# Performance work log

Measured on AMD Instinct MI355X. Metric: run time of the kernel, lower is better.

Reference implementation:

```python
import jax, jax.numpy as jnp
import numpy as np

B, N, D = 4, 8192, 512
L, W, S = 64, 64, 32  # num_tokens, win_size, stride


def setup_inputs() -> dict:
    key = jax.random.key(0)
    ks = jax.random.split(key, 12)
    inp = {
        "feats": jax.random.normal(ks[0], (B, N, D), jnp.float32),
        "coords": jax.random.normal(ks[1], (B, N, 2), jnp.float32) * 100.0,
        "mask": jnp.zeros((B, N), dtype=bool),
        "z": jax.random.normal(ks[2], (L, D), jnp.float32) * 0.02,
        "Wq": jax.random.normal(ks[3], (D, D), jnp.float32) * 0.01,
        "Wk": jax.random.normal(ks[4], (D, D), jnp.float32) * 0.01,
        "Wv": jax.random.normal(ks[5], (D, D), jnp.float32) * 0.01,
        "W1": jax.random.normal(ks[6], (D, 2), jnp.float32) * 0.05,
        "b1": jnp.zeros((D,), jnp.float32),
        "W2": jax.random.normal(ks[7], (D, D), jnp.float32) * 0.01,
        "b2": jnp.zeros((D,), jnp.float32),
        "Wo": jax.random.normal(ks[8], (D, D), jnp.float32) * 0.01,
        "bo": jnp.zeros((D,), jnp.float32),
    }
    return inp


def reference(feats, coords, mask, z, Wq, Wk, Wv, W1, b1, W2, b2, Wo, bo):
    # mask is all-False: every token valid, N_valid == N, segments are
    # contiguous blocks of P = N // L tokens (seg_id = floor(i*L/N)).
    Bz, Nn, Dd = feats.shape
    Ll = z.shape[0]
    P = Nn // Ll  # tokens per segment

    # LayerNorm over feature dim (no affine, eps=1e-5 as in F.layer_norm)
    mu = feats.mean(-1, keepdims=True)
    var = feats.var(-1, keepdims=True)
    f_ln = (feats - mu) * jax.lax.rsqrt(var + 1e-5)

    # per-sample coordinate normalization (torch std is unbiased, ddof=1)
    c_mu = coords.mean(1, keepdims=True)
    c_sd = coords.std(1, keepdims=True, ddof=1) + 1e-8
    c_n = (coords - c_mu) / c_sd

    f_seg = f_ln.reshape(Bz, Ll, P, Dd)
    c_seg = c_n.reshape(Bz, Ll, P, 2)

    # static sliding windows within each segment (last window may be partial)
    starts = np.arange(0, P, S)                      # [nw]
    idx = starts[:, None] + np.arange(W)[None, :]    # [nw, W]
    valid = jnp.asarray(idx < P)                     # [nw, W] bool
    idx_c = np.minimum(idx, P - 1)
    cnt = valid.sum(-1).astype(feats.dtype)          # [nw]

    f_win = f_seg[:, :, idx_c]                       # [B,L,nw,W,D]
    c_win = c_seg[:, :, idx_c]                       # [B,L,nw,W,2]

    vmask = valid.astype(feats.dtype)[None, None, :, :, None]
    c_mean = (c_win * vmask).sum(3) / cnt[None, None, :, None]   # [B,L,nw,2]
    pos_in = c_win - c_mean[:, :, :, None, :]
    h = jax.nn.relu(jnp.einsum('blnwc,dc->blnwd', pos_in, W1) + b1)
    pos_bias = jnp.einsum('blnwd,ed->blnwe', h, W2) + b2

    q = z @ Wq.T                                     # [L,D]
    k = jnp.einsum('blnwd,ed->blnwe', f_win, Wk) + pos_bias
    v = jnp.einsum('blnwd,ed->blnwe', f_win, Wv)

    temperature = jnp.sqrt(jnp.asarray(Dd, feats.dtype))
    logits = jnp.einsum('ld,blnwd->blnw', q, k) / temperature
    logits = jnp.clip(logits, -10.0, 10.0)
    logits = jnp.where(valid[None, None], logits, -jnp.inf)
    attn = jax.nn.softmax(logits, axis=-1)           # [B,L,nw,W]

    z_win = jnp.einsum('blnw,blnwd->blnd', attn, v)  # [B,L,nw,D]
    z_l = z_win.mean(2)                              # average over windows
    return z_l @ Wo.T + bo                           # [B,L,D]
```

## Files before the change

kernel.cpp:

```cpp
#include <hip/hip_runtime.h>

#define Bz 4
#define Nn 8192
#define Dd 512
#define Ll 64
#define Pp 128
#define Ww 64
#define Ss 32
#define NW 4

__global__ __launch_bounds__(256) void pre_k(
    const float* __restrict__ coords,
    const float* __restrict__ z,  const float* __restrict__ Wq,
    const float* __restrict__ Wk, const float* __restrict__ W2,
    const float* __restrict__ b2,
    const float* __restrict__ Wv, const float* __restrict__ Wo,
    float* __restrict__ cstats,
    float* __restrict__ QK, float* __restrict__ G,
    float* __restrict__ sqk4, float* __restrict__ qb2,
    float* __restrict__ WvoT) {
    __shared__ float smem[64 * 68 + 64 * 36];
    int bid = blockIdx.x, tid = threadIdx.x;
    int wv = tid >> 6, lane = tid & 63;

    if (bid < 256) {
        int l = bid & 63, ch = bid >> 6;
        float* qs  = smem;
        float* pq  = smem + 512;
        float* pg  = smem + 1536;
        float* red = smem + 2560;

        float zr[8];
        {
            const float4* zp = (const float4*)&z[(size_t)l * Dd + lane * 8];
            float4 z0 = zp[0], z1 = zp[1];
            zr[0] = z0.x; zr[1] = z0.y; zr[2] = z0.z; zr[3] = z0.w;
            zr[4] = z1.x; zr[5] = z1.y; zr[6] = z1.z; zr[7] = z1.w;
        }
        for (int i = 0; i < 128; i += 2) {
            int d0 = wv * 128 + i;
            const float4* r0 = (const float4*)&Wq[(size_t)d0 * Dd];
            const float4* r1 = (const float4*)&Wq[(size_t)(d0 + 1) * Dd];
            float4 a0 = r0[lane * 2], a1 = r0[lane * 2 + 1];
            float4 b0 = r1[lane * 2], b1 = r1[lane * 2 + 1];
            float s0 = a0.x * zr[0] + a0.y * zr[1] + a0.z * zr[2] + a0.w * zr[3]
                     + a1.x * zr[4] + a1.y * zr[5] + a1.z * zr[6] + a1.w * zr[7];
            float s1 = b0.x * zr[0] + b0.y * zr[1] + b0.z * zr[2] + b0.w * zr[3]
                     + b1.x * zr[4] + b1.y * zr[5] + b1.z * zr[6] + b1.w * zr[7];
            for (int o = 32; o > 0; o >>= 1) { s0 += __shfl_xor(s0, o); s1 += __shfl_xor(s1, o); }
            if (lane == 0) { qs[d0] = s0; qs[d0 + 1] = s1; }
        }
        __syncthreads();
        if (ch == 0) {
            float p = qs[tid] * b2[tid] + qs[tid + 256] * b2[tid + 256];
            for (int o = 32; o > 0; o >>= 1) p += __shfl_xor(p, o);
            if (lane == 0) red[4 + wv] = p;
        }
        {
            int qd = tid & 31, h = tid >> 5;
            int cb = ch * 128 + qd * 4;
            float4 aq = make_float4(0.f, 0.f, 0.f, 0.f);
            float4 ag = make_float4(0.f, 0.f, 0.f, 0.f);
            for (int e = h * 64; e < h * 64 + 64; ++e) {
                float qe = qs[e];
                float4 wk = *(const float4*)&Wk[(size_t)e * Dd + cb];
                float4 w2 = *(const float4*)&W2[(size_t)e * Dd + cb];
                aq.x = fmaf(qe, wk.x, aq.x); aq.y = fmaf(qe, wk.y, aq.y);
                aq.z = fmaf(qe, wk.z, aq.z); aq.w = fmaf(qe, wk.w, aq.w);
                ag.x = fmaf(qe, w2.x, ag.x); ag.y = fmaf(qe, w2.y, ag.y);
                ag.z = fmaf(qe, w2.z, ag.z); ag.w = fmaf(qe, w2.w, ag.w);
            }
            *(float4*)&pq[h * 128 + qd * 4] = aq;
            *(float4*)&pg[h * 128 + qd * 4] = ag;
        }
        __syncthreads();
        if (tid < 128) {
            float vq = 0.f, vg = 0.f;
#pragma unroll
            for (int hh = 0; hh < 8; ++hh) { vq += pq[hh * 128 + tid]; vg += pg[hh * 128 + tid]; }
            QK[(size_t)l * Dd + ch * 128 + tid] = vq;
            G [(size_t)l * Dd + ch * 128 + tid] = vg;
            float s = vq;
            for (int o = 32; o > 0; o >>= 1) s += __shfl_xor(s, o);
            if (lane == 0) red[wv] = s;
        }
        __syncthreads();
        if (tid == 0) sqk4[ch * 64 + l] = red[0] + red[1];
        if (ch == 0 && tid == 32) qb2[l] = red[4] + red[5] + red[6] + red[7];
    } else if (bid < 384) {
        int wb = bid - 256;
        int m0 = (wb >> 4) * 64;
        int n0 = (wb & 15) * 32;
        float (*As)[68] = (float (*)[68])smem;
        float (*Bs)[36] = (float (*)[36])(smem + 64 * 68);
        int tx = tid & 31, ty = tid >> 5;
        float acc[8] = {0.f, 0.f, 0.f, 0.f, 0.f, 0.f, 0.f, 0.f};
        for (int c0 = 0; c0 < Dd; c0 += 64) {
            int r = tid >> 4, c4 = (tid & 15) * 4;
#pragma unroll
            for (int i = 0; i < 4; ++i) {
                int cc = r + 16 * i;
                float4 v = *(const float4*)&Wv[(size_t)(c0 + cc) * Dd + m0 + c4];
                As[c4 + 0][cc] = v.x; As[c4 + 1][cc] = v.y;
                As[c4 + 2][cc] = v.z; As[c4 + 3][cc] = v.w;
            }
#pragma unroll
            for (int i = 0; i < 2; ++i) {
                int nn = r + 16 * i;
                float4 v = *(const float4*)&Wo[(size_t)(n0 + nn) * Dd + c0 + c4];
                Bs[c4 + 0][nn] = v.x; Bs[c4 + 1][nn] = v.y;
                Bs[c4 + 2][nn] = v.z; Bs[c4 + 3][nn] = v.w;
            }
            __syncthreads();
#pragma unroll 16
            for (int kk = 0; kk < 64; ++kk) {
                float bv = Bs[kk][tx];
#pragma unroll
                for (int i = 0; i < 8; ++i)
                    acc[i] = fmaf(As[ty + 8 * i][kk], bv, acc[i]);
            }
            __syncthreads();
        }
#pragma unroll
        for (int i = 0; i < 8; ++i)
            WvoT[(size_t)(m0 + ty + 8 * i) * Dd + n0 + tx] = acc[i];
    } else {
        int b = bid - 384;
        double sx = 0, sy = 0, sxx = 0, syy = 0;
        const float4* cp = (const float4*)(coords + (size_t)b * Nn * 2);
        for (int i = tid; i < Nn / 2; i += 256) {
            float4 v = cp[i];
            sx  += (double)v.x + (double)v.z;
            sy  += (double)v.y + (double)v.w;
            sxx += (double)v.x * v.x + (double)v.z * v.z;
            syy += (double)v.y * v.y + (double)v.w * v.w;
        }
        for (int o = 32; o > 0; o >>= 1) {
            sx  += __shfl_down(sx,  o); sy  += __shfl_down(sy,  o);
            sxx += __shfl_down(sxx, o); syy += __shfl_down(syy, o);
        }
        double* dred = (double*)smem;
        if (lane == 0) {
            dred[wv * 4 + 0] = sx;  dred[wv * 4 + 1] = sy;
            dred[wv * 4 + 2] = sxx; dred[wv * 4 + 3] = syy;
        }
        __syncthreads();
        if (tid == 0) {
            double tx = 0, ty = 0, txx = 0, tyy = 0;
            for (int i = 0; i < 4; ++i) {
                tx += dred[i * 4 + 0]; ty += dred[i * 4 + 1];
                txx += dred[i * 4 + 2]; tyy += dred[i * 4 + 3];
            }
            const double N = (double)Nn;
            double mux = tx / N, muy = ty / N;
            double vx = (txx - N * mux * mux) / (N - 1.0);
            double vy = (tyy - N * muy * muy) / (N - 1.0);
            cstats[b * 4 + 0] = (float)mux;
            cstats[b * 4 + 1] = (float)muy;
            cstats[b * 4 + 2] = (float)sqrt(vx) + 1e-8f;
            cstats[b * 4 + 3] = (float)sqrt(vy) + 1e-8f;
        }
    }
}

__global__ __launch_bounds__(512) void attn2(
    const float* __restrict__ feats, const float* __restrict__ coords,
    const float* __restrict__ cstats,
    const float* __restrict__ QKm, const float* __restrict__ Gm,
    const float* __restrict__ sqk4, const float* __restrict__ qb2,
    const float* __restrict__ W1, const float* __restrict__ b1,
    const float* __restrict__ WvoT, const float* __restrict__ bo,
    float* __restrict__ out) {
    __shared__ float  qk_s[Dd];
    __shared__ float4 wpack[Dd];
    __shared__ float  scx[Pp], scy[Pp];
    __shared__ float  smu[Pp], srs[Pp], sa[Pp];
    __shared__ float  shs[NW * Ww];
    __shared__ float  sar[NW][Ww];
    __shared__ float  swt[Pp];
    __shared__ float  scm[8];
    __shared__ float  s2red[NW];
    __shared__ float  soff;
    __shared__ float  spart[4][Dd];
    __shared__ float  fm_s[Dd];

    int bx = blockIdx.x;
    int l = bx & 63, b = bx >> 6;
    int tid = threadIdx.x;
    int wv = tid >> 6, lane = tid & 63;

    qk_s[tid]  = QKm[l * Dd + tid];
    wpack[tid] = make_float4(W1[2 * tid], W1[2 * tid + 1], b1[tid], Gm[l * Dd + tid]);
    if (tid < Pp) {
        int row = bx * Pp + tid;
        float x = coords[(size_t)row * 2], y = coords[(size_t)row * 2 + 1];
        scx[tid] = (x - cstats[b * 4 + 0]) / cstats[b * 4 + 2];
        scy[tid] = (y - cstats[b * 4 + 1]) / cstats[b * 4 + 3];
    }
    float sqk_l = sqk4[l] + sqk4[64 + l] + sqk4[128 + l] + sqk4[192 + l];
    float qb2_l = qb2[l];
    __syncthreads();

    if (wv < 4) {
        int n = wv, w = lane;
        int nv = (n == 3) ? 32 : 64;
        float cx = (w < nv) ? scx[n * Ss + w] : 0.f;
        float cy = (w < nv) ? scy[n * Ss + w] : 0.f;
        for (int o = 32; o > 0; o >>= 1) { cx += __shfl_xor(cx, o); cy += __shfl_xor(cy, o); }
        if (lane == 0) { scm[n] = cx / (float)nv; scm[4 + n] = cy / (float)nv; }
    }

    const float* fbase = feats + (size_t)bx * Pp * Dd;
    float4 q0 = ((const float4*)qk_s)[lane];
    float4 q1 = ((const float4*)qk_s)[lane + 64];
#pragma unroll 2
    for (int i = 0; i < 16; ++i) {
        int r = wv * 16 + i;
        const float4* fr = (const float4*)(fbase + (size_t)r * Dd);
        float4 v0 = fr[lane];
        float4 v1 = fr[lane + 64];
        float s  = v0.x + v0.y + v0.z + v0.w + v1.x + v1.y + v1.z + v1.w;
        float ss = v0.x * v0.x + v0.y * v0.y + v0.z * v0.z + v0.w * v0.w
                 + v1.x * v1.x + v1.y * v1.y + v1.z * v1.z + v1.w * v1.w;
        float a  = v0.x * q0.x + v0.y * q0.y + v0.z * q0.z + v0.w * q0.w
                 + v1.x * q1.x + v1.y * q1.y + v1.z * q1.z + v1.w * q1.w;
        for (int o = 32; o > 0; o >>= 1) {
            s += __shfl_xor(s, o); ss += __shfl_xor(ss, o); a += __shfl_xor(a, o);
        }
        if (lane == 0) {
            float mu  = s * (1.f / (float)Dd);
            float var = ss * (1.f / (float)Dd) - mu * mu;
            smu[r] = mu; srs[r] = 1.f / sqrtf(var + 1e-5f); sa[r] = a;
        }
    }
    __syncthreads();

    {
        int s = tid >> 1, half = tid & 1;
        int n = s >> 6, w = s & 63;
        int nv = (n == 3) ? 32 : 64;
        float hs = 0.f;
        if (w < nv) {
            int p = n * Ss + w;
            float px = scx[p] - scm[n], py = scy[p] - scm[4 + n];
            int d0 = half * 256;
#pragma unroll 4
            for (int d = d0; d < d0 + 256; ++d) {
                float4 c = wpack[d];
                hs = fmaf(c.w, fmaxf(fmaf(c.x, px, fmaf(c.y, py, c.z)), 0.f), hs);
            }
        }
        hs += __shfl_xor(hs, 1);
        if (half == 0) shs[s] = hs;
    }
    __syncthreads();

    const float invtemp = 0.04419417382415922f;
    if (wv < 4) {
        int n = wv, w = lane;
        int nv = (n == 3) ? 32 : 64;
        int p = n * Ss + ((w < nv) ? w : 0);
        float lg = -1e30f;
        if (w < nv) {
            lg = (srs[p] * (sa[p] - smu[p] * sqk_l) + shs[n * Ww + w] + qb2_l) * invtemp;
            lg = fminf(fmaxf(lg, -10.f), 10.f);
        }
        float m = lg;
        for (int o = 32; o > 0; o >>= 1) m = fmaxf(m, __shfl_xor(m, o));
        float e = (w < nv) ? expf(lg - m) : 0.f;
        float ssum = e;
        for (int o = 32; o > 0; o >>= 1) ssum += __shfl_xor(ssum, o);
        float ar = (w < nv) ? (e / ssum) * srs[p] : 0.f;
        sar[n][w] = ar;
        float t2 = (w < nv) ? ar * smu[p] : 0.f;
        for (int o = 32; o > 0; o >>= 1) t2 += __shfl_xor(t2, o);
        if (lane == 0) s2red[n] = t2;
    }
    __syncthreads();

    if (tid < Pp) {
        int p = tid;
        int na = (p >> 5) - 1, nb = (p >> 5);
        float wt = 0.f;
        if (na >= 0 && na <= 3) wt += sar[na][p - na * Ss];
        if (nb <= 3)            wt += sar[nb][p - nb * Ss];
        swt[p] = wt;
    }
    if (tid == 0) soff = 0.25f * (s2red[0] + s2red[1] + s2red[2] + s2red[3]);
    __syncthreads();

    {
        int g = tid >> 7, c4 = tid & 127;
        const float4* f4 = (const float4*)fbase;
        float4 acc = make_float4(0.f, 0.f, 0.f, 0.f);
#pragma unroll 4
        for (int p = g; p < Pp; p += 4) {
            float wt = swt[p];
            float4 v = f4[p * 128 + c4];
            acc.x = fmaf(wt, v.x, acc.x);
            acc.y = fmaf(wt, v.y, acc.y);
            acc.z = fmaf(wt, v.z, acc.z);
            acc.w = fmaf(wt, v.w, acc.w);
        }
        *(float4*)&spart[g][c4 * 4] = acc;
    }
    __syncthreads();
    fm_s[tid] = 0.25f * (spart[0][tid] + spart[1][tid] + spart[2][tid] + spart[3][tid]) - soff;
    __syncthreads();

    {
        int cq = (tid & 127) * 4, h = tid >> 7;
        float4 acc = make_float4(0.f, 0.f, 0.f, 0.f);
#pragma unroll 4
        for (int e = h * 128; e < h * 128 + 128; ++e) {
            float fe = fm_s[e];
            float4 w = *(const float4*)&WvoT[(size_t)e * Dd + cq];
            acc.x = fmaf(fe, w.x, acc.x);
            acc.y = fmaf(fe, w.y, acc.y);
            acc.z = fmaf(fe, w.z, acc.z);
            acc.w = fmaf(fe, w.w, acc.w);
        }
        *(float4*)&spart[h][cq] = acc;
    }
    __syncthreads();
    out[(size_t)bx * Dd + tid] = bo[tid]
        + spart[0][tid] + spart[1][tid] + spart[2][tid] + spart[3][tid];
}

extern "C" void kernel_launch(void* const* d_in, const int* in_sizes, int n_in,
                              void* d_out, int out_size, void* d_ws, size_t ws_size,
                              hipStream_t stream) {
    const float* feats  = (const float*)d_in[0];
    const float* coords = (const float*)d_in[1];
    const float* z  = (const float*)d_in[3];
    const float* Wq = (const float*)d_in[4];
    const float* Wk = (const float*)d_in[5];
    const float* Wv = (const float*)d_in[6];
    const float* W1 = (const float*)d_in[7];
    const float* b1 = (const float*)d_in[8];
    const float* W2 = (const float*)d_in[9];
    const float* b2 = (const float*)d_in[10];
    const float* Wo = (const float*)d_in[11];
    const float* bo = (const float*)d_in[12];
    float* out = (float*)d_out;

    float* ws = (float*)d_ws;
    float* cstats = ws;
    float* QK     = ws + 16;
    float* G      = QK + Ll * Dd;
    float* sqk4   = G + Ll * Dd;
    float* qb2    = sqk4 + 256;
    float* WvoT   = qb2 + Ll;

    pre_k<<<388, 256, 0, stream>>>(coords, z, Wq, Wk, W2, b2, Wv, Wo,
                                   cstats, QK, G, sqk4, qb2, WvoT);

    attn2<<<Bz * Ll, 512, 0, stream>>>(feats, coords, cstats,
                                       QK, G, sqk4, qb2, W1, b1,
                                       WvoT, bo, out);
}
```

Before: 183.9 us.

## Precompute Wq·Wk and Wq·W2 products, keep feature rows in registers

The query-key projection is re-associated. Instead of computing q = z·Wq^T per token and then q·Wk, pre1 builds the weight products Wq^T·Wk, Wq^T·W2 and b2·Wq in tiled GEMM blocks, and a new qkg_k kernel applies z to them. In attn2 each block loads its 128×512 feature slab into registers once and reuses it for both the LayerNorm/dot pass and the weighted-sum pass, so the second global read of feats goes away. This adds a third launch and a large per-thread register footprint, which risks spills or lower occupancy.

New measurement: 199.6 us. 1.09x slower.

```diff
diff --git a/kernel.cpp b/kernel.cpp
--- a/kernel.cpp
+++ b/kernel.cpp
@@ -9,107 +9,56 @@
 #define Ss 32
 #define NW 4
 
-__global__ __launch_bounds__(256) void pre_k(
-    const float* __restrict__ coords,
-    const float* __restrict__ z,  const float* __restrict__ Wq,
-    const float* __restrict__ Wk, const float* __restrict__ W2,
-    const float* __restrict__ b2,
+__global__ __launch_bounds__(256) void pre1(
+    const float* __restrict__ coords, const float* __restrict__ b2,
+    const float* __restrict__ Wq, const float* __restrict__ Wk,
+    const float* __restrict__ W2,
     const float* __restrict__ Wv, const float* __restrict__ Wo,
     float* __restrict__ cstats,
-    float* __restrict__ QK, float* __restrict__ G,
-    float* __restrict__ sqk4, float* __restrict__ qb2,
-    float* __restrict__ WvoT) {
-    __shared__ float smem[64 * 68 + 64 * 36];
+    float* __restrict__ M1, float* __restrict__ M2,
+    float* __restrict__ WvoT, float* __restrict__ vb8) {
+    __shared__ float As[64][65];
+    __shared__ float Bs[64][36];
+    __shared__ float b2s[64];
+    __shared__ double dred[16];
     int bid = blockIdx.x, tid = threadIdx.x;
     int wv = tid >> 6, lane = tid & 63;
 
-    if (bid < 256) {
-        int l = bid & 63, ch = bid >> 6;
-        float* qs  = smem;
-        float* pq  = smem + 512;
-        float* pg  = smem + 1536;
-        float* red = smem + 2560;
-
-        float zr[8];
-        {
-            const float4* zp = (const float4*)&z[(size_t)l * Dd + lane * 8];
-            float4 z0 = zp[0], z1 = zp[1];
-            zr[0] = z0.x; zr[1] = z0.y; zr[2] = z0.z; zr[3] = z0.w;
-            zr[4] = z1.x; zr[5] = z1.y; zr[6] = z1.z; zr[7] = z1.w;
-        }
-        for (int i = 0; i < 128; i += 2) {
-            int d0 = wv * 128 + i;
-            const float4* r0 = (const float4*)&Wq[(size_t)d0 * Dd];
-            const float4* r1 = (const float4*)&Wq[(size_t)(d0 + 1) * Dd];
-            float4 a0 = r0[lane * 2], a1 = r0[lane * 2 + 1];
-            float4 b0 = r1[lane * 2], b1 = r1[lane * 2 + 1];
-            float s0 = a0.x * zr[0] + a0.y * zr[1] + a0.z * zr[2] + a0.w * zr[3]
-                     + a1.x * zr[4] + a1.y * zr[5] + a1.z * zr[6] + a1.w * zr[7];
-            float s1 = b0.x * zr[0] + b0.y * zr[1] + b0.z * zr[2] + b0.w * zr[3]
-                     + b1.x * zr[4] + b1.y * zr[5] + b1.z * zr[6] + b1.w * zr[7];
-            for (int o = 32; o > 0; o >>= 1) { s0 += __shfl_xor(s0, o); s1 += __shfl_xor(s1, o); }
-            if (lane == 0) { qs[d0] = s0; qs[d0 + 1] = s1; }
-        }
-        __syncthreads();
-        if (ch == 0) {
-            float p = qs[tid] * b2[tid] + qs[tid + 256] * b2[tid + 256];
-            for (int o = 32; o > 0; o >>= 1) p += __shfl_xor(p, o);
-            if (lane == 0) red[4 + wv] = p;
-        }
-        {
-            int qd = tid & 31, h = tid >> 5;
-            int cb = ch * 128 + qd * 4;
-            float4 aq = make_float4(0.f, 0.f, 0.f, 0.f);
-            float4 ag = make_float4(0.f, 0.f, 0.f, 0.f);
-            for (int e = h * 64; e < h * 64 + 64; ++e) {
-                float qe = qs[e];
-                float4 wk = *(const float4*)&Wk[(size_t)e * Dd + cb];
-                float4 w2 = *(const float4*)&W2[(size_t)e * Dd + cb];
-                aq.x = fmaf(qe, wk.x, aq.x); aq.y = fmaf(qe, wk.y, aq.y);
-                aq.z = fmaf(qe, wk.z, aq.z); aq.w = fmaf(qe, wk.w, aq.w);
-                ag.x = fmaf(qe, w2.x, ag.x); ag.y = fmaf(qe, w2.y, ag.y);
-                ag.z = fmaf(qe, w2.z, ag.z); ag.w = fmaf(qe, w2.w, ag.w);
-            }
-            *(float4*)&pq[h * 128 + qd * 4] = aq;
-            *(float4*)&pg[h * 128 + qd * 4] = ag;
-        }
-        __syncthreads();
-        if (tid < 128) {
-            float vq = 0.f, vg = 0.f;
-#pragma unroll
-            for (int hh = 0; hh < 8; ++hh) { vq += pq[hh * 128 + tid]; vg += pg[hh * 128 + tid]; }
-            QK[(size_t)l * Dd + ch * 128 + tid] = vq;
-            G [(size_t)l * Dd + ch * 128 + tid] = vg;
-            float s = vq;
-            for (int o = 32; o > 0; o >>= 1) s += __shfl_xor(s, o);
-            if (lane == 0) red[wv] = s;
-        }
-        __syncthreads();
-        if (tid == 0) sqk4[ch * 64 + l] = red[0] + red[1];
-        if (ch == 0 && tid == 32) qb2[l] = red[4] + red[5] + red[6] + red[7];
-    } else if (bid < 384) {
-        int wb = bid - 256;
+    if (bid < 384) {
+        int role = bid >> 7;
+        int wb = bid & 127;
         int m0 = (wb >> 4) * 64;
         int n0 = (wb & 15) * 32;
-        float (*As)[68] = (float (*)[68])smem;
-        float (*Bs)[36] = (float (*)[36])(smem + 64 * 68);
+        const float* Amat = (role == 2) ? Wv : Wq;
+        const float* Bmat = (role == 0) ? Wk : (role == 1) ? W2 : Wo;
+        float* Cmat = (role == 0) ? M1 : (role == 1) ? M2 : WvoT;
         int tx = tid & 31, ty = tid >> 5;
         float acc[8] = {0.f, 0.f, 0.f, 0.f, 0.f, 0.f, 0.f, 0.f};
-        for (int c0 = 0; c0 < Dd; c0 += 64) {
+        for (int k0 = 0; k0 < Dd; k0 += 64) {
             int r = tid >> 4, c4 = (tid & 15) * 4;
 #pragma unroll
             for (int i = 0; i < 4; ++i) {
-                int cc = r + 16 * i;
-                float4 v = *(const float4*)&Wv[(size_t)(c0 + cc) * Dd + m0 + c4];
-                As[c4 + 0][cc] = v.x; As[c4 + 1][cc] = v.y;
-                As[c4 + 2][cc] = v.z; As[c4 + 3][cc] = v.w;
+                int kk = r + 16 * i;
+                float4 v = *(const float4*)&Amat[(size_t)(k0 + kk) * Dd + m0 + c4];
+                As[c4 + 0][kk] = v.x; As[c4 + 1][kk] = v.y;
+                As[c4 + 2][kk] = v.z; As[c4 + 3][kk] = v.w;
             }
-#pragma unroll
-            for (int i = 0; i < 2; ++i) {
-                int nn = r + 16 * i;
-                float4 v = *(const float4*)&Wo[(size_t)(n0 + nn) * Dd + c0 + c4];
-                Bs[c4 + 0][nn] = v.x; Bs[c4 + 1][nn] = v.y;
-                Bs[c4 + 2][nn] = v.z; Bs[c4 + 3][nn] = v.w;
+            if (role == 2) {
+#pragma unroll
+                for (int i = 0; i < 2; ++i) {
+                    int nn = r + 16 * i;
+                    float4 v = *(const float4*)&Bmat[(size_t)(n0 + nn) * Dd + k0 + c4];
+                    Bs[c4 + 0][nn] = v.x; Bs[c4 + 1][nn] = v.y;
+                    Bs[c4 + 2][nn] = v.z; Bs[c4 + 3][nn] = v.w;
+                }
+            } else {
+                int kr = tid >> 3, c8 = (tid & 7) * 4;
+#pragma unroll
+                for (int i = 0; i < 2; ++i) {
+                    int kk = kr + 32 * i;
+                    float4 v = *(const float4*)&Bmat[(size_t)(k0 + kk) * Dd + n0 + c8];
+                    *(float4*)&Bs[kk][c8] = v;
+                }
             }
             __syncthreads();
 #pragma unroll 16
@@ -123,9 +72,23 @@
         }
 #pragma unroll
         for (int i = 0; i < 8; ++i)
-            WvoT[(size_t)(m0 + ty + 8 * i) * Dd + n0 + tx] = acc[i];
+            Cmat[(size_t)(m0 + ty + 8 * i) * Dd + n0 + tx] = acc[i];
+    } else if (bid < 392) {
+        int j = bid - 384;
+        if (tid < 64) b2s[tid] = b2[j * 64 + tid];
+        __syncthreads();
+        float a0 = 0.f, a1 = 0.f;
+#pragma unroll 4
+        for (int ee = 0; ee < 64; ++ee) {
+            int e = j * 64 + ee;
+            float be = b2s[ee];
+            a0 = fmaf(be, Wq[(size_t)e * Dd + tid], a0);
+            a1 = fmaf(be, Wq[(size_t)e * Dd + tid + 256], a1);
+        }
+        vb8[j * Dd + tid] = a0;
+        vb8[j * Dd + tid + 256] = a1;
     } else {
-        int b = bid - 384;
+        int b = bid - 392;
         double sx = 0, sy = 0, sxx = 0, syy = 0;
         const float4* cp = (const float4*)(coords + (size_t)b * Nn * 2);
         for (int i = tid; i < Nn / 2; i += 256) {
@@ -139,7 +102,6 @@
             sx  += __shfl_down(sx,  o); sy  += __shfl_down(sy,  o);
             sxx += __shfl_down(sxx, o); syy += __shfl_down(syy, o);
         }
-        double* dred = (double*)smem;
         if (lane == 0) {
             dred[wv * 4 + 0] = sx;  dred[wv * 4 + 1] = sy;
             dred[wv * 4 + 2] = sxx; dred[wv * 4 + 3] = syy;
@@ -161,6 +123,68 @@
             cstats[b * 4 + 3] = (float)sqrt(vy) + 1e-8f;
         }
     }
+}
+
+__global__ __launch_bounds__(256) void qkg_k(
+    const float* __restrict__ z, const float* __restrict__ M1,
+    const float* __restrict__ M2, const float* __restrict__ vb8,
+    float* __restrict__ QK, float* __restrict__ G,
+    float* __restrict__ sqk4, float* __restrict__ qb2) {
+    __shared__ float zs[Dd];
+    __shared__ float pq[8][128];
+    __shared__ float pg[8][128];
+    __shared__ float red[8];
+    int bid = blockIdx.x, tid = threadIdx.x;
+    int l = bid & 63, ch = bid >> 6;
+    int wv = tid >> 6, lane = tid & 63;
+
+    zs[tid]       = z[(size_t)l * Dd + tid];
+    zs[tid + 256] = z[(size_t)l * Dd + tid + 256];
+    __syncthreads();
+
+    if (ch == 0) {
+        float vba = 0.f, vbb = 0.f;
+#pragma unroll
+        for (int j = 0; j < 8; ++j) {
+            vba += vb8[j * Dd + tid];
+            vbb += vb8[j * Dd + tid + 256];
+        }
+        float p = zs[tid] * vba + zs[tid + 256] * vbb;
+        for (int o = 32; o > 0; o >>= 1) p += __shfl_xor(p, o);
+        if (lane == 0) red[4 + wv] = p;
+    }
+
+    {
+        int qd = tid & 31, h = tid >> 5;
+        int cb = ch * 128 + qd * 4;
+        float4 aq = make_float4(0.f, 0.f, 0.f, 0.f);
+        float4 ag = make_float4(0.f, 0.f, 0.f, 0.f);
+        for (int d = h * 64; d < h * 64 + 64; ++d) {
+            float zd = zs[d];
+            float4 m1 = *(const float4*)&M1[(size_t)d * Dd + cb];
+            float4 m2 = *(const float4*)&M2[(size_t)d * Dd + cb];
+            aq.x = fmaf(zd, m1.x, aq.x); aq.y = fmaf(zd, m1.y, aq.y);
+            aq.z = fmaf(zd, m1.z, aq.z); aq.w = fmaf(zd, m1.w, aq.w);
+            ag.x = fmaf(zd, m2.x, ag.x); ag.y = fmaf(zd, m2.y, ag.y);
+            ag.z = fmaf(zd, m2.z, ag.z); ag.w = fmaf(zd, m2.w, ag.w);
+        }
+        *(float4*)&pq[h][qd * 4] = aq;
+        *(float4*)&pg[h][qd * 4] = ag;
+    }
+    __syncthreads();
+    if (tid < 128) {
+        float vq = 0.f, vg = 0.f;
+#pragma unroll
+        for (int hh = 0; hh < 8; ++hh) { vq += pq[hh][tid]; vg += pg[hh][tid]; }
+        QK[(size_t)l * Dd + ch * 128 + tid] = vq;
+        G [(size_t)l * Dd + ch * 128 + tid] = vg;
+        float s = vq;
+        for (int o = 32; o > 0; o >>= 1) s += __shfl_xor(s, o);
+        if (lane == 0) red[wv] = s;
+    }
+    __syncthreads();
+    if (tid == 0) sqk4[ch * 64 + l] = red[0] + red[1];
+    if (ch == 0 && tid == 32) qb2[l] = red[4] + red[5] + red[6] + red[7];
 }
 
 __global__ __launch_bounds__(512) void attn2(
@@ -181,13 +205,22 @@
     __shared__ float  scm[8];
     __shared__ float  s2red[NW];
     __shared__ float  soff;
-    __shared__ float  spart[4][Dd];
+    __shared__ float  red8[8][Dd];
     __shared__ float  fm_s[Dd];
 
     int bx = blockIdx.x;
     int l = bx & 63, b = bx >> 6;
     int tid = threadIdx.x;
     int wv = tid >> 6, lane = tid & 63;
+
+    const float* fbase = feats + (size_t)bx * Pp * Dd;
+    float4 f0[16], f1[16];
+#pragma unroll
+    for (int i = 0; i < 16; ++i) {
+        const float4* fr = (const float4*)(fbase + (size_t)(wv * 16 + i) * Dd);
+        f0[i] = fr[lane * 2];
+        f1[i] = fr[lane * 2 + 1];
+    }
 
     qk_s[tid]  = QKm[l * Dd + tid];
     wpack[tid] = make_float4(W1[2 * tid], W1[2 * tid + 1], b1[tid], Gm[l * Dd + tid]);
@@ -210,24 +243,26 @@
         if (lane == 0) { scm[n] = cx / (float)nv; scm[4 + n] = cy / (float)nv; }
     }
 
-    const float* fbase = feats + (size_t)bx * Pp * Dd;
-    float4 q0 = ((const float4*)qk_s)[lane];
-    float4 q1 = ((const float4*)qk_s)[lane + 64];
-#pragma unroll 2
+    float4 q0 = ((const float4*)qk_s)[lane * 2];
+    float4 q1 = ((const float4*)qk_s)[lane * 2 + 1];
+    float sP[16], ssP[16], aP[16];
+#pragma unroll
     for (int i = 0; i < 16; ++i) {
-        int r = wv * 16 + i;
-        const float4* fr = (const float4*)(fbase + (size_t)r * Dd);
-        float4 v0 = fr[lane];
-        float4 v1 = fr[lane + 64];
-        float s  = v0.x + v0.y + v0.z + v0.w + v1.x + v1.y + v1.z + v1.w;
-        float ss = v0.x * v0.x + v0.y * v0.y + v0.z * v0.z + v0.w * v0.w
-                 + v1.x * v1.x + v1.y * v1.y + v1.z * v1.z + v1.w * v1.w;
-        float a  = v0.x * q0.x + v0.y * q0.y + v0.z * q0.z + v0.w * q0.w
-                 + v1.x * q1.x + v1.y * q1.y + v1.z * q1.z + v1.w * q1.w;
+        float4 v0 = f0[i], v1 = f1[i];
+        sP[i]  = v0.x + v0.y + v0.z + v0.w + v1.x + v1.y + v1.z + v1.w;
+        ssP[i] = v0.x * v0.x + v0.y * v0.y + v0.z * v0.z + v0.w * v0.w
+               + v1.x * v1.x + v1.y * v1.y + v1.z * v1.z + v1.w * v1.w;
+        aP[i]  = v0.x * q0.x + v0.y * q0.y + v0.z * q0.z + v0.w * q0.w
+               + v1.x * q1.x + v1.y * q1.y + v1.z * q1.z + v1.w * q1.w;
+    }
+#pragma unroll
+    for (int i = 0; i < 16; ++i) {
+        float s = sP[i], ss = ssP[i], a = aP[i];
         for (int o = 32; o > 0; o >>= 1) {
             s += __shfl_xor(s, o); ss += __shfl_xor(ss, o); a += __shfl_xor(a, o);
         }
         if (lane == 0) {
+            int r = wv * 16 + i;
             float mu  = s * (1.f / (float)Dd);
             float var = ss * (1.f / (float)Dd) - mu * mu;
             smu[r] = mu; srs[r] = 1.f / sqrtf(var + 1e-5f); sa[r] = a;
@@ -290,22 +325,26 @@
     __syncthreads();
 
     {
-        int g = tid >> 7, c4 = tid & 127;
-        const float4* f4 = (const float4*)fbase;
-        float4 acc = make_float4(0.f, 0.f, 0.f, 0.f);
-#pragma unroll 4
-        for (int p = g; p < Pp; p += 4) {
-            float wt = swt[p];
-            float4 v = f4[p * 128 + c4];
-            acc.x = fmaf(wt, v.x, acc.x);
-            acc.y = fmaf(wt, v.y, acc.y);
-            acc.z = fmaf(wt, v.z, acc.z);
-            acc.w = fmaf(wt, v.w, acc.w);
-        }
-        *(float4*)&spart[g][c4 * 4] = acc;
-    }
-    __syncthreads();
-    fm_s[tid] = 0.25f * (spart[0][tid] + spart[1][tid] + spart[2][tid] + spart[3][tid]) - soff;
+        float4 a0 = make_float4(0.f, 0.f, 0.f, 0.f);
+        float4 a1 = make_float4(0.f, 0.f, 0.f, 0.f);
+#pragma unroll
+        for (int i = 0; i < 16; ++i) {
+            float wt = swt[wv * 16 + i];
+            a0.x = fmaf(wt, f0[i].x, a0.x); a0.y = fmaf(wt, f0[i].y, a0.y);
+            a0.z = fmaf(wt, f0[i].z, a0.z); a0.w = fmaf(wt, f0[i].w, a0.w);
+            a1.x = fmaf(wt, f1[i].x, a1.x); a1.y = fmaf(wt, f1[i].y, a1.y);
+            a1.z = fmaf(wt, f1[i].z, a1.z); a1.w = fmaf(wt, f1[i].w, a1.w);
+        }
+        *(float4*)&red8[wv][lane * 8]     = a0;
+        *(float4*)&red8[wv][lane * 8 + 4] = a1;
+    }
+    __syncthreads();
+    {
+        float v = 0.f;
+#pragma unroll
+        for (int w = 0; w < 8; ++w) v += red8[w][tid];
+        fm_s[tid] = 0.25f * v - soff;
+    }
     __syncthreads();
 
     {
@@ -320,11 +359,11 @@
             acc.z = fmaf(fe, w.z, acc.z);
             acc.w = fmaf(fe, w.w, acc.w);
         }
-        *(float4*)&spart[h][cq] = acc;
+        *(float4*)&red8[h][cq] = acc;
     }
     __syncthreads();
     out[(size_t)bx * Dd + tid] = bo[tid]
-        + spart[0][tid] + spart[1][tid] + spart[2][tid] + spart[3][tid];
+        + red8[0][tid] + red8[1][tid] + red8[2][tid] + red8[3][tid];
 }
 
 extern "C" void kernel_launch(void* const* d_in, const int* in_sizes, int n_in,
@@ -346,15 +385,18 @@
 
     float* ws = (float*)d_ws;
     float* cstats = ws;
-    float* QK     = ws + 16;
+    float* M1     = ws + 16;
+    float* M2     = M1 + Dd * Dd;
+    float* WvoT   = M2 + Dd * Dd;
+    float* vb8    = WvoT + Dd * Dd;
+    float* QK     = vb8 + 8 * Dd;
     float* G      = QK + Ll * Dd;
     float* sqk4   = G + Ll * Dd;
     float* qb2    = sqk4 + 256;
-    float* WvoT   = qb2 + Ll;
-
-    pre_k<<<388, 256, 0, stream>>>(coords, z, Wq, Wk, W2, b2, Wv, Wo,
-                                   cstats, QK, G, sqk4, qb2, WvoT);
-
+
+    pre1<<<396, 256, 0, stream>>>(coords, b2, Wq, Wk, W2, Wv, Wo,
+                                  cstats, M1, M2, WvoT, vb8);
+    qkg_k<<<256, 256, 0, stream>>>(z, M1, M2, vb8, QK, G, sqk4, qb2);
     attn2<<<Bz * Ll, 512, 0, stream>>>(feats, coords, cstats,
                                        QK, G, sqk4, qb2, W1, b1,
                                        WvoT, bo, out);
```
